# Optimization experiments

Hardware: AMD Instinct MI355X
Metric: run time of the kernel (lower is better)

The kernel has to match this reference:

```python
import jax, jax.numpy as jnp
import numpy as np

NUM_HEADS = 8
NUM_GROUPS = 32
EPS = 1e-5


def group_norm(x, gamma, beta):
    # x: (B, C, N)
    B, C, N = x.shape
    xg = x.reshape(B, NUM_GROUPS, (C // NUM_GROUPS) * N)
    mean = xg.mean(axis=-1, keepdims=True)
    var = xg.var(axis=-1, keepdims=True)
    xg = (xg - mean) * jax.lax.rsqrt(var + EPS)
    x = xg.reshape(B, C, N)
    return x * gamma[None, :, None] + beta[None, :, None]


def setup_inputs() -> dict:
    key = jax.random.key(0)
    ks = jax.random.split(key, 7)
    B, C, H, W = 16, 512, 32, 32
    return {
        "x": jax.random.normal(ks[0], (B, C, H, W), dtype=jnp.float32),
        "gamma": jax.random.uniform(ks[1], (C,), dtype=jnp.float32, minval=0.5, maxval=1.5),
        "beta": jax.random.normal(ks[2], (C,), dtype=jnp.float32) * 0.1,
        "w_qkv": jax.random.normal(ks[3], (3 * C, C), dtype=jnp.float32) * 0.02,
        "b_qkv": jax.random.normal(ks[4], (3 * C,), dtype=jnp.float32) * 0.01,
        "w_proj": jax.random.normal(ks[5], (C, C), dtype=jnp.float32) * 0.02,
        "b_proj": jax.random.normal(ks[6], (C,), dtype=jnp.float32) * 0.01,
    }


def reference(x, gamma, beta, w_qkv, b_qkv, w_proj, b_proj):
    B, C, Hs, Ws = x.shape
    N = Hs * Ws
    x3 = x.reshape(B, C, N)
    xn = group_norm(x3, gamma, beta)
    # 1x1 Conv1d == channel-wise linear: (3C, C) x (B, C, N) -> (B, 3C, N)
    qkv = jnp.einsum('oc,bcn->bon', w_qkv, xn) + b_qkv[None, :, None]
    ch = C // NUM_HEADS
    qkv = qkv.reshape(B * NUM_HEADS, 3 * ch, N)
    q, k, v = jnp.split(qkv, 3, axis=1)  # each (B*H, ch, N)
    scale = ch ** (-0.25)
    w = jnp.einsum('bct,bcs->bts', q * scale, k * scale)  # (B*H, N, N)
    w = jax.nn.softmax(w.astype(jnp.float32), axis=-1).astype(q.dtype)
    h = jnp.einsum('bts,bcs->bct', w, v)  # (B*H, ch, N)
    h = h.reshape(B, C, N)
    h = jnp.einsum('oc,bcn->bon', w_proj, h) + b_proj[None, :, None]
    return (x3 + h).reshape(B, C, Hs, Ws)
```

## Files before the change

kernel.cpp:

```cpp
#include <hip/hip_runtime.h>
#include <stdint.h>

typedef unsigned short u16;
typedef float f32x4 __attribute__((ext_vector_type(4)));
typedef short bf16x8 __attribute__((ext_vector_type(8)));

#define DEV __device__ __forceinline__

DEV u16 f2bf(float f) {
  union { float f; unsigned int u; } v; v.f = f;
  unsigned int u = v.u;
  u = (u + 0x7FFFu + ((u >> 16) & 1u)) >> 16;
  return (u16)u;
}

DEV float exp2_(float x) {
#if __has_builtin(__builtin_amdgcn_exp2f)
  return __builtin_amdgcn_exp2f(x);
#else
  return exp2f(x);
#endif
}

DEV unsigned int cvt_pk_bf16(float lo, float hi) {
  unsigned int r;
  asm("v_cvt_pk_bf16_f32 %0, %1, %2" : "=v"(r) : "v"(lo), "v"(hi));
  return r;
}

typedef __attribute__((address_space(1))) const unsigned int* gas_t;
typedef __attribute__((address_space(3))) unsigned int* las_t;
DEV void gload16(const void* g, void* l) {
  __builtin_amdgcn_global_load_lds((gas_t)g, (las_t)l, 16, 0, 0);
}

DEV f32x4 zf4() { f32x4 z = {0.f, 0.f, 0.f, 0.f}; return z; }

static constexpr float QK_SCALE = 0.35355339059327373f;
static constexpr float LOG2E    = 1.4426950408889634f;

static constexpr size_t OFF_WQKV  = 0;
static constexpr size_t OFF_WPROJ = 1572864;
static constexpr size_t OFF_XNT   = 2097152;
static constexpr size_t OFF_Q     = 18874368;
static constexpr size_t OFF_K     = 35651584;
static constexpr size_t OFF_V     = 52428800;
static constexpr size_t OFF_HT    = 69206016;

__global__ __launch_bounds__(256) void prep_kernel(const float* __restrict__ x,
                                                   const float* __restrict__ gamma,
                                                   const float* __restrict__ beta,
                                                   const float* __restrict__ wqkv,
                                                   const float* __restrict__ wproj,
                                                   u16* __restrict__ xnt,
                                                   u16* __restrict__ dq, u16* __restrict__ dp) {
  int tid = threadIdx.x;
  int blk = blockIdx.x;
  if (blk >= 512) {
    int i = (blk - 512) * 256 + tid;
    const float4* src; u16* dst; int j;
    if (i < 196608) { src = (const float4*)wqkv;  dst = dq; j = i; }
    else            { src = (const float4*)wproj; dst = dp; j = i - 196608; }
    float4 v = src[j];
    uint2 o; o.x = cvt_pk_bf16(v.x, v.y); o.y = cvt_pk_bf16(v.z, v.w);
    *(uint2*)(dst + (size_t)j * 4) = o;
    return;
  }
  __shared__ float rs[4], rss[4], bcast[2];
  int b = blk >> 5, g = blk & 31;
  const float4* p = (const float4*)(x + (size_t)blk * 16384);
  float4 v[16];
  float s = 0.f, ss = 0.f;
  #pragma unroll
  for (int it = 0; it < 16; ++it) {
    v[it] = p[it * 256 + tid];
    s  += v[it].x + v[it].y + v[it].z + v[it].w;
    ss += v[it].x*v[it].x + v[it].y*v[it].y + v[it].z*v[it].z + v[it].w*v[it].w;
  }
  #pragma unroll
  for (int off = 32; off > 0; off >>= 1) {
    s  += __shfl_down(s, off);
    ss += __shfl_down(ss, off);
  }
  int wid = tid >> 6;
  if ((tid & 63) == 0) { rs[wid] = s; rss[wid] = ss; }
  __syncthreads();
  if (tid == 0) {
    s  = rs[0] + rs[1] + rs[2] + rs[3];
    ss = rss[0] + rss[1] + rss[2] + rss[3];
    float mean = s * (1.f / 16384.f);
    float var  = ss * (1.f / 16384.f) - mean * mean;
    bcast[0] = mean;
    bcast[1] = rsqrtf(var + 1e-5f);
  }
  __syncthreads();
  float mean = bcast[0], rstd = bcast[1];
  float ga[16], be[16];
  #pragma unroll
  for (int it = 0; it < 16; ++it) {
    float gm = gamma[g*16 + it];
    ga[it] = gm * rstd;
    be[it] = beta[g*16 + it] - mean * ga[it];
  }
  u16* dst = xnt + ((size_t)(b*1024 + tid*4)) * 512 + g*16;
  #pragma unroll
  for (int k = 0; k < 4; ++k) {
    unsigned int w[8];
    #pragma unroll
    for (int j = 0; j < 8; ++j) {
      float e, o;
      switch (k) {
        case 0: e = v[2*j].x; o = v[2*j+1].x; break;
        case 1: e = v[2*j].y; o = v[2*j+1].y; break;
        case 2: e = v[2*j].z; o = v[2*j+1].z; break;
        default: e = v[2*j].w; o = v[2*j+1].w; break;
      }
      w[j] = cvt_pk_bf16(e*ga[2*j] + be[2*j], o*ga[2*j+1] + be[2*j+1]);
    }
    uint4 lo; lo.x = w[0]; lo.y = w[1]; lo.z = w[2]; lo.w = w[3];
    uint4 hi; hi.x = w[4]; hi.y = w[5]; hi.z = w[6]; hi.w = w[7];
    *(uint4*)(dst + (size_t)k*512)     = lo;
    *(uint4*)(dst + (size_t)k*512 + 8) = hi;
  }
}

template<int EPI>
__global__ __launch_bounds__(256) void gemm_kernel(const u16* __restrict__ A,
                                                   const u16* __restrict__ Bm,
                                                   const float* __restrict__ bias,
                                                   u16* __restrict__ Qp, u16* __restrict__ Kp,
                                                   u16* __restrict__ Vp,
                                                   const float* __restrict__ xres,
                                                   float* __restrict__ outp) {
  __shared__ u16 lds[4 * 128 * 64];
  int tid = threadIdx.x, lane = tid & 63, wid = tid >> 6;
  int tl = lane & 15, g = lane >> 4;
  int wm = wid >> 1, wn = wid & 1;
  int tM = blockIdx.y, tN = blockIdx.x;
  int o0 = tM * 128, n0 = tN * 128;
  f32x4 acc[4][4];
  #pragma unroll
  for (int i = 0; i < 4; ++i)
    #pragma unroll
    for (int j = 0; j < 4; ++j) acc[i][j] = zf4();

  int rl = lane >> 3, sg = lane & 7;
  const u16* Ag = A  + (size_t)(o0 + wid*32 + rl) * 512 + ((sg ^ rl) << 3);
  const u16* Bg = Bm + (size_t)(n0 + wid*32 + rl) * 512 + ((sg ^ rl) << 3);
  int wofs = wid*32*64;

#define STAGE_GEMM(buf, kt)                                                     \
  {                                                                             \
    u16* Ad = lds + (buf)*16384 + wofs;                                         \
    u16* Bd = lds + (buf)*16384 + 8192 + wofs;                                  \
    _Pragma("unroll")                                                           \
    for (int q = 0; q < 4; ++q) {                                               \
      gload16(Ag + (size_t)q*8*512 + (kt)*64, Ad + q*8*64);                     \
      gload16(Bg + (size_t)q*8*512 + (kt)*64, Bd + q*8*64);                     \
    }                                                                           \
  }

  STAGE_GEMM(0, 0);
  __syncthreads();
  for (int kt = 0; kt < 8; ++kt) {
    int cur = kt & 1;
    if (kt < 7) STAGE_GEMM(cur ^ 1, kt + 1);
    const u16* Als = lds + cur*16384;
    const u16* Bls = lds + cur*16384 + 8192;
    #pragma unroll
    for (int kk = 0; kk < 2; ++kk) {
      bf16x8 av[4], bv[4];
      #pragma unroll
      for (int mi = 0; mi < 4; ++mi)
        av[mi] = *(const bf16x8*)&Als[(wm*64 + mi*16 + tl)*64 + (((kk*4 + g) ^ (tl & 7)) << 3)];
      #pragma unroll
      for (int ni = 0; ni < 4; ++ni)
        bv[ni] = *(const bf16x8*)&Bls[(wn*64 + ni*16 + tl)*64 + (((kk*4 + g) ^ (tl & 7)) << 3)];
      #pragma unroll
      for (int mi = 0; mi < 4; ++mi)
        #pragma unroll
        for (int ni = 0; ni < 4; ++ni)
          acc[mi][ni] = __builtin_amdgcn_mfma_f32_16x16x32_bf16(av[mi], bv[ni], acc[mi][ni], 0, 0, 0);
    }
    __syncthreads();
  }
#undef STAGE_GEMM

  if (EPI == 1) {
    #pragma unroll
    for (int mi = 0; mi < 4; ++mi) {
      int mb = mi*16 + (g << 2);
      float4 bs = *(const float4*)&bias[o0 + wm*64 + mb];
      const float* bsf = (const float*)&bs;
      #pragma unroll
      for (int ni = 0; ni < 4; ++ni) {
        int n_g = n0 + wn*64 + ni*16 + tl;
        int bb = n_g >> 10, n = n_g & 1023;
        #pragma unroll
        for (int rr = 0; rr < 4; ++rr) {
          int o_g = o0 + wm*64 + mb + rr;
          size_t oi = (((size_t)(bb*512 + o_g)) << 10) + n;
          outp[oi] = acc[mi][ni][rr] + bsf[rr] + xres[oi];
        }
      }
    }
    return;
  }

  int a = 2*tM + wm;
  int head = a / 3;
  int sect = a - head*3;
  float sc = (sect == 0) ? QK_SCALE : (sect == 1 ? QK_SCALE * LOG2E : 1.f);
  u16* wl = lds + wid * (64*64);
  #pragma unroll
  for (int mi = 0; mi < 4; ++mi) {
    int mb = mi*16 + (g << 2);
    float4 bs = *(const float4*)&bias[o0 + wm*64 + mb];
    const float* bsf = (const float*)&bs;
    #pragma unroll
    for (int ni = 0; ni < 4; ++ni) {
      int nl = ni*16 + tl;
      #pragma unroll
      for (int rr = 0; rr < 4; ++rr) {
        float val = (acc[mi][ni][rr] + bsf[rr]) * sc;
        int ml = mb + rr;
        if (sect < 2) wl[nl*64 + (ml ^ ((nl & 7) << 3))] = f2bf(val);
        else          wl[ml*64 + (nl ^ ((ml & 7) << 3))] = f2bf(val);
      }
    }
  }
  int n_wb = n0 + wn*64;
  int bb = n_wb >> 10, nn0 = n_wb & 1023;
  int bh = bb*8 + head;
  #pragma unroll
  for (int p = 0; p < 8; ++p) {
    int row = p*8 + (lane >> 3), sgg = lane & 7;
    uint4 v = *(const uint4*)&wl[row*64 + ((sgg ^ (row & 7)) << 3)];
    if (sect == 0)
      *(uint4*)(Qp + (((size_t)bh) << 16) + (size_t)(nn0 + row)*64 + sgg*8) = v;
    else if (sect == 1)
      *(uint4*)(Kp + (((size_t)bh) << 16) + (size_t)(nn0 + row)*64 + sgg*8) = v;
    else
      *(uint4*)(Vp + (((size_t)bh) << 16) + (size_t)row*1024 + nn0 + sgg*8) = v;
  }
}

__global__ __launch_bounds__(256, 4) void attn_kernel(const u16* __restrict__ Qp,
                                                      const u16* __restrict__ Kp,
                                                      const u16* __restrict__ Vp,
                                                      u16* __restrict__ Hp) {
  __shared__ u16 KVls[2 * 2 * 4096];
  __shared__ u16 Pls[4 * 32 * 64];
  int tid = threadIdx.x, lane = tid & 63, w = tid >> 6;
  int id = blockIdx.x;
  int bh = ((id >> 6) << 3) | (id & 7);
  int tblk = (id >> 3) & 7;
  int t0 = tblk * 128 + w * 32;
  size_t hb = ((size_t)bh) << 16;
  int tl = lane & 15, g = lane >> 4;

  bf16x8 bq[2][2];
  #pragma unroll
  for (int tf = 0; tf < 2; ++tf)
    #pragma unroll
    for (int kk = 0; kk < 2; ++kk)
      bq[tf][kk] = *(const bf16x8*)(Qp + hb + (size_t)(t0 + tf*16 + tl)*64 + kk*32 + g*8);

  f32x4 oacc[4][2];
  #pragma unroll
  for (int ci = 0; ci < 4; ++ci)
    #pragma unroll
    for (int tf = 0; tf < 2; ++tf) oacc[ci][tf] = zf4();
  float l_run[2] = {0.f, 0.f};
  u16* pw = Pls + w * (32 * 64);
  int xsw = (tl & 7) << 3;

  int r8 = lane >> 3, sg8 = lane & 7;
  int swz = ((sg8 ^ r8) << 3);

#define STAGE_KV(buf, sbase)                                                        \
  { _Pragma("unroll")                                                               \
    for (int q = 0; q < 2; ++q) {                                                   \
      int row = q*32 + w*8 + r8;                                                    \
      gload16(Kp + hb + (size_t)(sbase + row)*64 + swz,                             \
              KVls + (buf)*8192 + (q*256 + w*64)*8);                                \
      gload16(Vp + hb + (size_t)row*1024 + (sbase) + swz,                           \
              KVls + (buf)*8192 + 4096 + (q*256 + w*64)*8);                         \
    } }

  STAGE_KV(0, 0);
  __syncthreads();
  for (int it = 0; it < 16; ++it) {
    int cur = it & 1;
    if (it < 15) STAGE_KV(cur ^ 1, (it + 1) * 64);
    const u16* Kls = KVls + cur*8192;
    const u16* Vls = KVls + cur*8192 + 4096;

    f32x4 sfr[2][4];
    #pragma unroll
    for (int tf = 0; tf < 2; ++tf)
      #pragma unroll
      for (int ni = 0; ni < 4; ++ni) sfr[tf][ni] = zf4();
    __builtin_amdgcn_s_setprio(1);
    #pragma unroll
    for (int kk = 0; kk < 2; ++kk) {
      bf16x8 ak[4];
      #pragma unroll
      for (int ni = 0; ni < 4; ++ni)
        ak[ni] = *(const bf16x8*)&Kls[(ni*16 + tl)*64 + ((((kk*4 + g) << 3)) ^ xsw)];
      #pragma unroll
      for (int tf = 0; tf < 2; ++tf)
        #pragma unroll
        for (int ni = 0; ni < 4; ++ni)
          sfr[tf][ni] = __builtin_amdgcn_mfma_f32_16x16x32_bf16(ak[ni], bq[tf][kk], sfr[tf][ni], 0, 0, 0);
    }
    __builtin_amdgcn_s_setprio(0);

    #pragma unroll
    for (int tf = 0; tf < 2; ++tf) {
      int trow = tf*16 + tl;
      int rsw = (trow & 7) << 3;
      float lt = 0.f;
      #pragma unroll
      for (int ni = 0; ni < 4; ++ni) {
        float p0 = exp2_(sfr[tf][ni][0]);
        float p1 = exp2_(sfr[tf][ni][1]);
        float p2 = exp2_(sfr[tf][ni][2]);
        float p3 = exp2_(sfr[tf][ni][3]);
        lt += (p0 + p1) + (p2 + p3);
        uint2 pkv;
        pkv.x = cvt_pk_bf16(p0, p1);
        pkv.y = cvt_pk_bf16(p2, p3);
        *(uint2*)&pw[trow*64 + ((ni*16 + g*4) ^ rsw)] = pkv;
      }
      l_run[tf] += lt;
    }

    __builtin_amdgcn_s_setprio(1);
    #pragma unroll
    for (int kk = 0; kk < 2; ++kk) {
      bf16x8 av[4];
      #pragma unroll
      for (int ci = 0; ci < 4; ++ci)
        av[ci] = *(const bf16x8*)&Vls[(ci*16 + tl)*64 + ((((kk*4 + g) << 3)) ^ xsw)];
      #pragma unroll
      for (int tf = 0; tf < 2; ++tf) {
        int trow = tf*16 + tl;
        bf16x8 bp = *(const bf16x8*)&pw[trow*64 + (((kk*4 + g) << 3) ^ ((trow & 7) << 3))];
        #pragma unroll
        for (int ci = 0; ci < 4; ++ci)
          oacc[ci][tf] = __builtin_amdgcn_mfma_f32_16x16x32_bf16(av[ci], bp, oacc[ci][tf], 0, 0, 0);
      }
    }
    __builtin_amdgcn_s_setprio(0);
    __syncthreads();
  }
#undef STAGE_KV

  #pragma unroll
  for (int tf = 0; tf < 2; ++tf) {
    float l = l_run[tf];
    l += __shfl_xor(l, 16);
    l += __shfl_xor(l, 32);
    float inv = 1.f / l;
    int trow = tf*16 + tl;
    int rsw = (trow & 7) << 3;
    #pragma unroll
    for (int ci = 0; ci < 4; ++ci) {
      uint2 pkv;
      pkv.x = cvt_pk_bf16(oacc[ci][tf][0]*inv, oacc[ci][tf][1]*inv);
      pkv.y = cvt_pk_bf16(oacc[ci][tf][2]*inv, oacc[ci][tf][3]*inv);
      *(uint2*)&pw[trow*64 + ((ci*16 + g*4) ^ rsw)] = pkv;
    }
  }
  int b = bh >> 3, head = bh & 7;
  #pragma unroll
  for (int p = 0; p < 4; ++p) {
    int row = p*8 + (lane >> 3), sgg = lane & 7;
    uint4 v = *(const uint4*)&pw[row*64 + ((sgg ^ (row & 7)) << 3)];
    *(uint4*)(Hp + ((size_t)(b*1024 + t0 + row))*512 + head*64 + sgg*8) = v;
  }
}

extern "C" void kernel_launch(void* const* d_in, const int* in_sizes, int n_in,
                              void* d_out, int out_size, void* d_ws, size_t ws_size,
                              hipStream_t stream) {
  const float* x     = (const float*)d_in[0];
  const float* gamma = (const float*)d_in[1];
  const float* beta  = (const float*)d_in[2];
  const float* wqkv  = (const float*)d_in[3];
  const float* bqkv  = (const float*)d_in[4];
  const float* wproj = (const float*)d_in[5];
  const float* bproj = (const float*)d_in[6];
  float* out = (float*)d_out;
  char* ws = (char*)d_ws;
  u16* wqkv_bf  = (u16*)(ws + OFF_WQKV);
  u16* wproj_bf = (u16*)(ws + OFF_WPROJ);
  u16* xnt = (u16*)(ws + OFF_XNT);
  u16* Qp  = (u16*)(ws + OFF_Q);
  u16* Kp  = (u16*)(ws + OFF_K);
  u16* Vp  = (u16*)(ws + OFF_V);
  u16* Hp  = (u16*)(ws + OFF_HT);

  prep_kernel<<<1536, 256, 0, stream>>>(x, gamma, beta, wqkv, wproj, xnt, wqkv_bf, wproj_bf);
  gemm_kernel<0><<<dim3(128, 12), 256, 0, stream>>>(wqkv_bf, xnt, bqkv, Qp, Kp, Vp, nullptr, nullptr);
  attn_kernel<<<1024, 256, 0, stream>>>(Qp, Kp, Vp, Hp);
  gemm_kernel<1><<<dim3(128, 4), 256, 0, stream>>>(wproj_bf, Hp, bproj, nullptr, nullptr, nullptr, x, out);
}
```

Measured before the change: 204.3 us.

## Replace double-buffered async KV staging with single-buffer synchronous loads

The attention kernel's K/V tiles were prefetched into a double buffer with direct global-to-LDS async loads, overlapping the next tile's load with the current tile's compute. This replaces that with one buffer filled each iteration through plain register loads and LDS stores, followed by a barrier. It halves K/V shared memory, which may allow more resident blocks. In exchange, load latency is no longer hidden behind the MFMA work.

```diff
diff --git a/kernel.cpp b/kernel.cpp
--- a/kernel.cpp
+++ b/kernel.cpp
@@ -249,7 +249,8 @@
                                                       const u16* __restrict__ Kp,
                                                       const u16* __restrict__ Vp,
                                                       u16* __restrict__ Hp) {
-  __shared__ u16 KVls[2 * 2 * 4096];
+  __shared__ u16 Kls[64 * 64];
+  __shared__ u16 Vls[64 * 64];
   __shared__ u16 Pls[4 * 32 * 64];
   int tid = threadIdx.x, lane = tid & 63, w = tid >> 6;
   int id = blockIdx.x;
@@ -273,28 +274,18 @@
     for (int tf = 0; tf < 2; ++tf) oacc[ci][tf] = zf4();
   float l_run[2] = {0.f, 0.f};
   u16* pw = Pls + w * (32 * 64);
+  int sr = tid >> 3, sseg = tid & 7;
   int xsw = (tl & 7) << 3;
 
-  int r8 = lane >> 3, sg8 = lane & 7;
-  int swz = ((sg8 ^ r8) << 3);
-
-#define STAGE_KV(buf, sbase)                                                        \
-  { _Pragma("unroll")                                                               \
-    for (int q = 0; q < 2; ++q) {                                                   \
-      int row = q*32 + w*8 + r8;                                                    \
-      gload16(Kp + hb + (size_t)(sbase + row)*64 + swz,                             \
-              KVls + (buf)*8192 + (q*256 + w*64)*8);                                \
-      gload16(Vp + hb + (size_t)row*1024 + (sbase) + swz,                           \
-              KVls + (buf)*8192 + 4096 + (q*256 + w*64)*8);                         \
-    } }
-
-  STAGE_KV(0, 0);
-  __syncthreads();
-  for (int it = 0; it < 16; ++it) {
-    int cur = it & 1;
-    if (it < 15) STAGE_KV(cur ^ 1, (it + 1) * 64);
-    const u16* Kls = KVls + cur*8192;
-    const u16* Vls = KVls + cur*8192 + 4096;
+  for (int s0 = 0; s0 < 1024; s0 += 64) {
+    #pragma unroll
+    for (int p = 0; p < 2; ++p) {
+      int row = p*32 + sr;
+      int woff = row*64 + ((sseg ^ (row & 7)) << 3);
+      *(uint4*)&Kls[woff] = *(const uint4*)(Kp + hb + (size_t)(s0 + row)*64 + sseg*8);
+      *(uint4*)&Vls[woff] = *(const uint4*)(Vp + hb + (size_t)row*1024 + s0 + sseg*8);
+    }
+    __syncthreads();
 
     f32x4 sfr[2][4];
     #pragma unroll
@@ -355,7 +346,6 @@
     __builtin_amdgcn_s_setprio(0);
     __syncthreads();
   }
-#undef STAGE_KV
 
   #pragma unroll
   for (int tf = 0; tf < 2; ++tf) {
```

New measurement: 189.2 us. 1.08x faster.
